# Kernel tuning notes

Hardware: AMD Instinct MI355X
Metric: run time of the kernel (lower is better)

The kernel has to match this reference:

```python
import jax, jax.numpy as jnp
import numpy as np

# opt hyperparameters (from init_kwargs)
L = 16        # number of multipath taps
M = 64        # number of subcarriers (FFT size for H_t)
N_PILOT = 2   # pilot symbols
V = 100.0     # velocity used for Doppler shift


def setup_inputs() -> dict:
    key = jax.random.key(0)
    k1, k2, k3, k4 = jax.random.split(key, 4)
    N, P, S, MK = 1024, 8, 14, 80
    SMK = S * MK  # 1120
    return {
        "input_real": jax.random.normal(k1, (N, P, SMK), dtype=jnp.float32),
        "input_imag": jax.random.normal(k2, (N, P, SMK), dtype=jnp.float32),
        "cof_real": jax.random.normal(k3, (N, P, L), dtype=jnp.float32),
        "cof_imag": jax.random.normal(k4, (N, P, L), dtype=jnp.float32),
        "Ns": 12,
    }


def reference(input_real, input_imag, cof_real, cof_imag, Ns):
    N, P, SMK = input_real.shape
    S = Ns + N_PILOT
    x = (input_real + 1j * input_imag).astype(jnp.complex64)   # (N,P,SMK)
    cof = (cof_real + 1j * cof_imag).astype(jnp.complex64)      # (N,P,L)

    # H_t: FFT of zero-padded channel taps along delay dim
    cof_zp = jnp.concatenate([cof, jnp.zeros((N, P, M - L), dtype=cof.dtype)], axis=-1)
    H_t = jnp.fft.fft(cof_zp, axis=-1)                          # (N,P,M)

    # Doppler phase shifts: shift[l,s] = exp(i * 2*pi*cos(angle_l)*fd * t_s)
    t = jnp.linspace(0.0, (S - 1) * (0.0005 / 14.0), S)         # (S,)
    carrier_freq = 3.0e9
    max_doppler = V / 3.0e8 * carrier_freq
    angles = jnp.linspace(0.0, 2.0 * np.pi, L)                  # (L,)
    phases = jnp.outer(2.0 * np.pi * jnp.cos(angles) * max_doppler, t)  # (L,S)
    shift = jnp.exp(1j * phases).astype(jnp.complex64)          # (L,S)

    # out[n,p,s,k] = sum_l x[n,p,s,k] * cof[n,p,l] * shift[l,s]
    # The sum over L factors out of the MK dim -> fused weight, avoiding the
    # (N,P,L,S,MK) broadcast intermediate the original materializes.
    weight = jnp.einsum('npl,ls->nps', cof, shift)              # (N,P,S)
    out = x.reshape(N, P, S, -1) * weight[..., None]            # (N,P,S,MK)
    output = out.reshape(N, P, SMK)
    return output, H_t
```

## Files before the change

kernel.cpp:

```cpp
#include <hip/hip_runtime.h>
#include <math.h>

#define L_TAPS 16
#define M_FFT  64
#define ROWS   4
#define SMAX   128

__global__ __launch_bounds__(256) void channel_fused(
    const float* __restrict__ xr, const float* __restrict__ xi,
    const float* __restrict__ cr, const float* __restrict__ ci,
    const int*   __restrict__ ns_ptr,
    float* __restrict__ out,
    int NP, int SMK)
{
    __shared__ float2 s_tw[M_FFT];
    __shared__ float  s_dop[L_TAPS];
    __shared__ float2 s_cof[ROWS][L_TAPS];
    __shared__ float2 s_w[ROWS * SMAX];

    const int tid  = threadIdx.x;
    const int S    = ns_ptr[0] + 2;
    const int MK   = SMK / S;
    const int row0 = blockIdx.x * ROWS;

    const float two_pi = 6.2831853071795864f;

    if (tid < M_FFT) {
        float sp, cp;
        __sincosf(-(float)tid * (two_pi / (float)M_FFT), &sp, &cp);
        s_tw[tid] = make_float2(cp, sp);
    } else if (tid < M_FFT + L_TAPS) {
        int l = tid - M_FFT;
        s_dop[l] = two_pi * __cosf((float)l * (two_pi / (float)(L_TAPS - 1)))
                 * (100.0f / 3.0e8f * 3.0e9f);
    } else if (tid >= 128 && tid < 128 + ROWS * L_TAPS) {
        int r = (tid - 128) >> 4, l = tid & 15;
        int npp = row0 + r;
        if (npp < NP)
            s_cof[r][l] = make_float2(cr[(size_t)npp * L_TAPS + l],
                                      ci[(size_t)npp * L_TAPS + l]);
    }
    __syncthreads();

    if (S <= SMAX) {
        const int l = tid & 15;
        for (int s = tid >> 4; s < S; s += 16) {
            float sp, cp;
            __sincosf(s_dop[l] * ((float)s * (0.0005f / 14.0f)), &sp, &cp);
            #pragma unroll
            for (int r = 0; r < ROWS; ++r) {
                float2 c = s_cof[r][l];
                float pr = c.x * cp - c.y * sp;
                float pi_ = c.x * sp + c.y * cp;
                #pragma unroll
                for (int off = 8; off; off >>= 1) {
                    pr  += __shfl_xor(pr,  off, 16);
                    pi_ += __shfl_xor(pi_, off, 16);
                }
                if (l == 0 && row0 + r < NP) s_w[r * S + s] = make_float2(pr, pi_);
            }
        }
    }

    {
        const int r = tid >> 6, m = tid & 63;
        const int npp = row0 + r;
        if (npp < NP) {
            float hr = 0.f;
            #pragma unroll
            for (int l = 0; l < L_TAPS; ++l) {
                float2 c = s_cof[r][l];
                float2 t = s_tw[(m * l) & (M_FFT - 1)];
                hr += c.x * t.x - c.y * t.y;
            }
            out[(size_t)NP * SMK + (size_t)npp * M_FFT + m] = hr;
        }
    }
    __syncthreads();

    const int rows_here = min(ROWS, NP - row0);
    if (S <= SMAX && (MK & 3) == 0 && (SMK & 3) == 0) {
        const int   mkq   = MK >> 2;
        const int   limit = (rows_here * SMK) >> 2;
        const size_t gb   = (size_t)row0 * (SMK >> 2);
        const float4* xr4 = (const float4*)xr + gb;
        const float4* xi4 = (const float4*)xi + gb;
        float4*       o4  = (float4*)out + gb;
        for (int v = tid; v < limit; v += 256) {
            float4 a = xr4[v];
            float4 b = xi4[v];
            float2 w = s_w[(unsigned)v / (unsigned)mkq];
            float4 r4;
            r4.x = a.x * w.x - b.x * w.y;
            r4.y = a.y * w.x - b.y * w.y;
            r4.z = a.z * w.x - b.z * w.y;
            r4.w = a.w * w.x - b.w * w.y;
            o4[v] = r4;
        }
    } else if (S <= SMAX) {
        const size_t gb = (size_t)row0 * SMK;
        const int limit = rows_here * SMK;
        for (int i = tid; i < limit; i += 256) {
            float2 w = s_w[(unsigned)i / (unsigned)MK];
            out[gb + i] = xr[gb + i] * w.x - xi[gb + i] * w.y;
        }
    } else {
        const size_t gb = (size_t)row0 * SMK;
        const int limit = rows_here * SMK;
        for (int i = tid; i < limit; i += 256) {
            int r = i / SMK, s = (i - r * SMK) / MK;
            float wr = 0.f, wi = 0.f;
            #pragma unroll
            for (int l = 0; l < L_TAPS; ++l) {
                float sp, cp;
                __sincosf(s_dop[l] * ((float)s * (0.0005f / 14.0f)), &sp, &cp);
                float2 c = s_cof[r][l];
                wr += c.x * cp - c.y * sp;
                wi += c.x * sp + c.y * cp;
            }
            out[gb + i] = xr[gb + i] * wr - xi[gb + i] * wi;
        }
    }
}

extern "C" void kernel_launch(void* const* d_in, const int* in_sizes, int n_in,
                              void* d_out, int out_size, void* d_ws, size_t ws_size,
                              hipStream_t stream) {
    const float* xr = (const float*)d_in[0];
    const float* xi = (const float*)d_in[1];
    const float* cr = (const float*)d_in[2];
    const float* ci = (const float*)d_in[3];
    const int*   ns = (const int*)  d_in[4];

    const int NP  = in_sizes[2] / L_TAPS;
    const int SMK = in_sizes[0] / NP;
    (void)d_ws; (void)ws_size; (void)out_size; (void)n_in;

    channel_fused<<<(NP + ROWS - 1) / ROWS, 256, 0, stream>>>(
        xr, xi, cr, ci, ns, (float*)d_out, NP, SMK);
}
```

Before: 25.59 us.

## Unroll streaming loop with nontemporal vector loads and per-thread weight computation

The main streaming loop is unrolled by four so each thread issues four independent vector loads of both input planes before computing. The loads and stores use nontemporal builtins to bypass cache retention. The Doppler weight computation moves from a shuffle-reduction across 16 lanes to a per-thread 16-tap loop on the upper half of the block, with the Doppler constants folded in at compile time. It also drops the shared Doppler table and restricts the fast path to full blocks. The risk is that the per-thread sincos loop lengthens the prologue before the barrier.

```diff
diff --git a/kernel.cpp b/kernel.cpp
--- a/kernel.cpp
+++ b/kernel.cpp
@@ -5,6 +5,8 @@
 #define M_FFT  64
 #define ROWS   4
 #define SMAX   128
+
+typedef float v4f __attribute__((ext_vector_type(4)));
 
 __global__ __launch_bounds__(256) void channel_fused(
     const float* __restrict__ xr, const float* __restrict__ xi,
@@ -14,7 +16,6 @@
     int NP, int SMK)
 {
     __shared__ float2 s_tw[M_FFT];
-    __shared__ float  s_dop[L_TAPS];
     __shared__ float2 s_cof[ROWS][L_TAPS];
     __shared__ float2 s_w[ROWS * SMAX];
 
@@ -22,49 +23,48 @@
     const int S    = ns_ptr[0] + 2;
     const int MK   = SMK / S;
     const int row0 = blockIdx.x * ROWS;
-
     const float two_pi = 6.2831853071795864f;
 
-    if (tid < M_FFT) {
-        float sp, cp;
-        __sincosf(-(float)tid * (two_pi / (float)M_FFT), &sp, &cp);
-        s_tw[tid] = make_float2(cp, sp);
-    } else if (tid < M_FFT + L_TAPS) {
-        int l = tid - M_FFT;
-        s_dop[l] = two_pi * __cosf((float)l * (two_pi / (float)(L_TAPS - 1)))
-                 * (100.0f / 3.0e8f * 3.0e9f);
-    } else if (tid >= 128 && tid < 128 + ROWS * L_TAPS) {
-        int r = (tid - 128) >> 4, l = tid & 15;
+    if (tid < ROWS * L_TAPS) {
+        int r = tid >> 4, l = tid & 15;
         int npp = row0 + r;
         if (npp < NP)
             s_cof[r][l] = make_float2(cr[(size_t)npp * L_TAPS + l],
                                       ci[(size_t)npp * L_TAPS + l]);
+    } else if (tid < 64 + M_FFT) {
+        int m = tid - 64;
+        float sp, cp;
+        __sincosf(-(float)m * (two_pi / (float)M_FFT), &sp, &cp);
+        s_tw[m] = make_float2(cp, sp);
     }
     __syncthreads();
 
-    if (S <= SMAX) {
-        const int l = tid & 15;
-        for (int s = tid >> 4; s < S; s += 16) {
-            float sp, cp;
-            __sincosf(s_dop[l] * ((float)s * (0.0005f / 14.0f)), &sp, &cp);
-            #pragma unroll
-            for (int r = 0; r < ROWS; ++r) {
-                float2 c = s_cof[r][l];
-                float pr = c.x * cp - c.y * sp;
-                float pi_ = c.x * sp + c.y * cp;
+    if (S <= SMAX && tid >= 128) {
+        for (int q = tid - 128; q < ROWS * S; q += 128) {
+            int r = q / S;
+            int s = q - r * S;
+            if (row0 + r < NP) {
+                float t = (float)s * (0.0005f / 14.0f);
+                float wr = 0.f, wi = 0.f;
                 #pragma unroll
-                for (int off = 8; off; off >>= 1) {
-                    pr  += __shfl_xor(pr,  off, 16);
-                    pi_ += __shfl_xor(pi_, off, 16);
+                for (int l = 0; l < L_TAPS; ++l) {
+                    float dop = two_pi
+                              * __cosf((float)l * (two_pi / (float)(L_TAPS - 1)))
+                              * 1000.0f;
+                    float sp, cp;
+                    __sincosf(dop * t, &sp, &cp);
+                    float2 c = s_cof[r][l];
+                    wr += c.x * cp - c.y * sp;
+                    wi += c.x * sp + c.y * cp;
                 }
-                if (l == 0 && row0 + r < NP) s_w[r * S + s] = make_float2(pr, pi_);
+                s_w[q] = make_float2(wr, wi);
             }
         }
     }
 
     {
-        const int r = tid >> 6, m = tid & 63;
-        const int npp = row0 + r;
+        int r = tid >> 6, m = tid & 63;
+        int npp = row0 + r;
         if (npp < NP) {
             float hr = 0.f;
             #pragma unroll
@@ -79,23 +79,49 @@
     __syncthreads();
 
     const int rows_here = min(ROWS, NP - row0);
-    if (S <= SMAX && (MK & 3) == 0 && (SMK & 3) == 0) {
-        const int   mkq   = MK >> 2;
-        const int   limit = (rows_here * SMK) >> 2;
-        const size_t gb   = (size_t)row0 * (SMK >> 2);
-        const float4* xr4 = (const float4*)xr + gb;
-        const float4* xi4 = (const float4*)xi + gb;
-        float4*       o4  = (float4*)out + gb;
-        for (int v = tid; v < limit; v += 256) {
-            float4 a = xr4[v];
-            float4 b = xi4[v];
-            float2 w = s_w[(unsigned)v / (unsigned)mkq];
-            float4 r4;
-            r4.x = a.x * w.x - b.x * w.y;
-            r4.y = a.y * w.x - b.y * w.y;
-            r4.z = a.z * w.x - b.z * w.y;
-            r4.w = a.w * w.x - b.w * w.y;
-            o4[v] = r4;
+    if (S <= SMAX && (MK & 3) == 0 && (SMK & 3) == 0 && rows_here == ROWS) {
+        const unsigned mkq = (unsigned)(MK >> 2);
+        const int nvr   = SMK >> 2;
+        const int limit = ROWS * nvr;
+        const size_t gb = (size_t)row0 * nvr;
+        const v4f* xr4 = (const v4f*)xr + gb;
+        const v4f* xi4 = (const v4f*)xi + gb;
+        v4f*       o4  = (v4f*)out + gb;
+        const int niters = limit >> 8;
+
+        int j = 0;
+        for (; j + 4 <= niters; j += 4) {
+            const int v0 = (j << 8) + tid, v1 = v0 + 256, v2 = v0 + 512, v3 = v0 + 768;
+            v4f a0 = __builtin_nontemporal_load(xr4 + v0);
+            v4f a1 = __builtin_nontemporal_load(xr4 + v1);
+            v4f a2 = __builtin_nontemporal_load(xr4 + v2);
+            v4f a3 = __builtin_nontemporal_load(xr4 + v3);
+            v4f b0 = __builtin_nontemporal_load(xi4 + v0);
+            v4f b1 = __builtin_nontemporal_load(xi4 + v1);
+            v4f b2 = __builtin_nontemporal_load(xi4 + v2);
+            v4f b3 = __builtin_nontemporal_load(xi4 + v3);
+            float2 w0 = s_w[(unsigned)v0 / mkq];
+            float2 w1 = s_w[(unsigned)v1 / mkq];
+            float2 w2 = s_w[(unsigned)v2 / mkq];
+            float2 w3 = s_w[(unsigned)v3 / mkq];
+            __builtin_nontemporal_store(a0 * w0.x - b0 * w0.y, o4 + v0);
+            __builtin_nontemporal_store(a1 * w1.x - b1 * w1.y, o4 + v1);
+            __builtin_nontemporal_store(a2 * w2.x - b2 * w2.y, o4 + v2);
+            __builtin_nontemporal_store(a3 * w3.x - b3 * w3.y, o4 + v3);
+        }
+        for (; j < niters; ++j) {
+            const int v = (j << 8) + tid;
+            v4f a = __builtin_nontemporal_load(xr4 + v);
+            v4f b = __builtin_nontemporal_load(xi4 + v);
+            float2 w = s_w[(unsigned)v / mkq];
+            __builtin_nontemporal_store(a * w.x - b * w.y, o4 + v);
+        }
+        const int t = (niters << 8) + tid;
+        if (t < limit) {
+            v4f a = __builtin_nontemporal_load(xr4 + t);
+            v4f b = __builtin_nontemporal_load(xi4 + t);
+            float2 w = s_w[(unsigned)t / mkq];
+            __builtin_nontemporal_store(a * w.x - b * w.y, o4 + t);
         }
     } else if (S <= SMAX) {
         const size_t gb = (size_t)row0 * SMK;
@@ -109,11 +135,15 @@
         const int limit = rows_here * SMK;
         for (int i = tid; i < limit; i += 256) {
             int r = i / SMK, s = (i - r * SMK) / MK;
+            float t = (float)s * (0.0005f / 14.0f);
             float wr = 0.f, wi = 0.f;
             #pragma unroll
             for (int l = 0; l < L_TAPS; ++l) {
+                float dop = two_pi
+                          * __cosf((float)l * (two_pi / (float)(L_TAPS - 1)))
+                          * 1000.0f;
                 float sp, cp;
-                __sincosf(s_dop[l] * ((float)s * (0.0005f / 14.0f)), &sp, &cp);
+                __sincosf(dop * t, &sp, &cp);
                 float2 c = s_cof[r][l];
                 wr += c.x * cp - c.y * sp;
                 wi += c.x * sp + c.y * cp;
```

New measurement: 24.60 us. 3.9% less time.

## Map one row per block with 320 threads and nontemporal vector I/O

Applied to the files above, without the earlier changes.

Restructures the kernel so each block handles a single (n,p) row: 280 threads each load one float4 of real and imaginary input up front, 64 threads compute the H_t FFT taps directly with sincos, and S threads compute per-symbol Doppler weights without shuffles. Loads are issued before the weight computation so memory latency overlaps the math, and nontemporal loads/stores are used for streaming data. This gives 8192 blocks instead of 2048 and removes shared twiddle/coef staging and one barrier. The cost is more blocks, repeated cof loads from global, and 40 idle lanes per block in the streaming phase.

```diff
diff --git a/kernel.cpp b/kernel.cpp
--- a/kernel.cpp
+++ b/kernel.cpp
@@ -3,120 +3,120 @@
 
 #define L_TAPS 16
 #define M_FFT  64
-#define ROWS   4
 #define SMAX   128
+#define BLOCK  320
 
-__global__ __launch_bounds__(256) void channel_fused(
+typedef float v4f __attribute__((ext_vector_type(4)));
+
+__global__ __launch_bounds__(BLOCK) void channel_fused(
     const float* __restrict__ xr, const float* __restrict__ xi,
     const float* __restrict__ cr, const float* __restrict__ ci,
     const int*   __restrict__ ns_ptr,
     float* __restrict__ out,
     int NP, int SMK)
 {
-    __shared__ float2 s_tw[M_FFT];
-    __shared__ float  s_dop[L_TAPS];
-    __shared__ float2 s_cof[ROWS][L_TAPS];
-    __shared__ float2 s_w[ROWS * SMAX];
+    __shared__ float2 s_w[SMAX];
 
-    const int tid  = threadIdx.x;
-    const int S    = ns_ptr[0] + 2;
-    const int MK   = SMK / S;
-    const int row0 = blockIdx.x * ROWS;
-
+    const int tid = threadIdx.x;
+    const int np  = blockIdx.x;
+    const int S   = ns_ptr[0] + 2;
+    const int MK  = SMK / S;
     const float two_pi = 6.2831853071795864f;
 
-    if (tid < M_FFT) {
-        float sp, cp;
-        __sincosf(-(float)tid * (two_pi / (float)M_FFT), &sp, &cp);
-        s_tw[tid] = make_float2(cp, sp);
-    } else if (tid < M_FFT + L_TAPS) {
-        int l = tid - M_FFT;
-        s_dop[l] = two_pi * __cosf((float)l * (two_pi / (float)(L_TAPS - 1)))
-                 * (100.0f / 3.0e8f * 3.0e9f);
-    } else if (tid >= 128 && tid < 128 + ROWS * L_TAPS) {
-        int r = (tid - 128) >> 4, l = tid & 15;
-        int npp = row0 + r;
-        if (npp < NP)
-            s_cof[r][l] = make_float2(cr[(size_t)npp * L_TAPS + l],
-                                      ci[(size_t)npp * L_TAPS + l]);
-    }
-    __syncthreads();
+    const float* crow = cr + (size_t)np * L_TAPS;
+    const float* cirow = ci + (size_t)np * L_TAPS;
 
-    if (S <= SMAX) {
-        const int l = tid & 15;
-        for (int s = tid >> 4; s < S; s += 16) {
-            float sp, cp;
-            __sincosf(s_dop[l] * ((float)s * (0.0005f / 14.0f)), &sp, &cp);
-            #pragma unroll
-            for (int r = 0; r < ROWS; ++r) {
-                float2 c = s_cof[r][l];
-                float pr = c.x * cp - c.y * sp;
-                float pi_ = c.x * sp + c.y * cp;
-                #pragma unroll
-                for (int off = 8; off; off >>= 1) {
-                    pr  += __shfl_xor(pr,  off, 16);
-                    pi_ += __shfl_xor(pi_, off, 16);
-                }
-                if (l == 0 && row0 + r < NP) s_w[r * S + s] = make_float2(pr, pi_);
-            }
+    const int nvr = SMK >> 2;
+    const bool fast = ((MK & 3) == 0) && ((SMK & 3) == 0) && (nvr <= BLOCK) && (S <= SMAX);
+
+    if (fast) {
+        const size_t gb = (size_t)np * nvr;
+        const bool act = tid < nvr;
+        v4f a, b;
+        if (act) {
+            a = __builtin_nontemporal_load((const v4f*)xr + gb + tid);
+            b = __builtin_nontemporal_load((const v4f*)xi + gb + tid);
         }
-    }
-
-    {
-        const int r = tid >> 6, m = tid & 63;
-        const int npp = row0 + r;
-        if (npp < NP) {
+        if (tid >= BLOCK - 64) {
+            const int m = tid - (BLOCK - 64);
             float hr = 0.f;
             #pragma unroll
             for (int l = 0; l < L_TAPS; ++l) {
-                float2 c = s_cof[r][l];
-                float2 t = s_tw[(m * l) & (M_FFT - 1)];
-                hr += c.x * t.x - c.y * t.y;
+                float sp, cp;
+                __sincosf((float)((m * l) & (M_FFT - 1)) * (two_pi / (float)M_FFT), &sp, &cp);
+                hr += crow[l] * cp + cirow[l] * sp;
             }
-            out[(size_t)NP * SMK + (size_t)npp * M_FFT + m] = hr;
+            __builtin_nontemporal_store(
+                hr, out + (size_t)NP * SMK + (size_t)np * M_FFT + m);
         }
+        if (tid < S) {
+            const float t = (float)tid * (0.0005f / 14.0f);
+            float wr = 0.f, wi = 0.f;
+            #pragma unroll
+            for (int l = 0; l < L_TAPS; ++l) {
+                float dop = two_pi * 1000.0f
+                          * __cosf((float)l * (two_pi / (float)(L_TAPS - 1)));
+                float sp, cp;
+                __sincosf(dop * t, &sp, &cp);
+                wr += crow[l] * cp - cirow[l] * sp;
+                wi += crow[l] * sp + cirow[l] * cp;
+            }
+            s_w[tid] = make_float2(wr, wi);
+        }
+        __syncthreads();
+        if (act) {
+            float2 w = s_w[(unsigned)tid / (unsigned)(MK >> 2)];
+            __builtin_nontemporal_store(a * w.x - b * w.y, (v4f*)out + gb + tid);
+        }
+        return;
     }
-    __syncthreads();
 
-    const int rows_here = min(ROWS, NP - row0);
-    if (S <= SMAX && (MK & 3) == 0 && (SMK & 3) == 0) {
-        const int   mkq   = MK >> 2;
-        const int   limit = (rows_here * SMK) >> 2;
-        const size_t gb   = (size_t)row0 * (SMK >> 2);
-        const float4* xr4 = (const float4*)xr + gb;
-        const float4* xi4 = (const float4*)xi + gb;
-        float4*       o4  = (float4*)out + gb;
-        for (int v = tid; v < limit; v += 256) {
-            float4 a = xr4[v];
-            float4 b = xi4[v];
-            float2 w = s_w[(unsigned)v / (unsigned)mkq];
-            float4 r4;
-            r4.x = a.x * w.x - b.x * w.y;
-            r4.y = a.y * w.x - b.y * w.y;
-            r4.z = a.z * w.x - b.z * w.y;
-            r4.w = a.w * w.x - b.w * w.y;
-            o4[v] = r4;
+    if (tid >= BLOCK - 64) {
+        const int m = tid - (BLOCK - 64);
+        float hr = 0.f;
+        #pragma unroll
+        for (int l = 0; l < L_TAPS; ++l) {
+            float sp, cp;
+            __sincosf((float)((m * l) & (M_FFT - 1)) * (two_pi / (float)M_FFT), &sp, &cp);
+            hr += crow[l] * cp + cirow[l] * sp;
         }
-    } else if (S <= SMAX) {
-        const size_t gb = (size_t)row0 * SMK;
-        const int limit = rows_here * SMK;
-        for (int i = tid; i < limit; i += 256) {
+        out[(size_t)NP * SMK + (size_t)np * M_FFT + m] = hr;
+    }
+    if (S <= SMAX) {
+        if (tid < S) {
+            const float t = (float)tid * (0.0005f / 14.0f);
+            float wr = 0.f, wi = 0.f;
+            #pragma unroll
+            for (int l = 0; l < L_TAPS; ++l) {
+                float dop = two_pi * 1000.0f
+                          * __cosf((float)l * (two_pi / (float)(L_TAPS - 1)));
+                float sp, cp;
+                __sincosf(dop * t, &sp, &cp);
+                wr += crow[l] * cp - cirow[l] * sp;
+                wi += crow[l] * sp + cirow[l] * cp;
+            }
+            s_w[tid] = make_float2(wr, wi);
+        }
+        __syncthreads();
+        const size_t gb = (size_t)np * SMK;
+        for (int i = tid; i < SMK; i += BLOCK) {
             float2 w = s_w[(unsigned)i / (unsigned)MK];
             out[gb + i] = xr[gb + i] * w.x - xi[gb + i] * w.y;
         }
     } else {
-        const size_t gb = (size_t)row0 * SMK;
-        const int limit = rows_here * SMK;
-        for (int i = tid; i < limit; i += 256) {
-            int r = i / SMK, s = (i - r * SMK) / MK;
+        const size_t gb = (size_t)np * SMK;
+        for (int i = tid; i < SMK; i += BLOCK) {
+            int s = i / MK;
+            float t = (float)s * (0.0005f / 14.0f);
             float wr = 0.f, wi = 0.f;
             #pragma unroll
             for (int l = 0; l < L_TAPS; ++l) {
+                float dop = two_pi * 1000.0f
+                          * __cosf((float)l * (two_pi / (float)(L_TAPS - 1)));
                 float sp, cp;
-                __sincosf(s_dop[l] * ((float)s * (0.0005f / 14.0f)), &sp, &cp);
-                float2 c = s_cof[r][l];
-                wr += c.x * cp - c.y * sp;
-                wi += c.x * sp + c.y * cp;
+                __sincosf(dop * t, &sp, &cp);
+                wr += crow[l] * cp - cirow[l] * sp;
+                wi += crow[l] * sp + cirow[l] * cp;
             }
             out[gb + i] = xr[gb + i] * wr - xi[gb + i] * wi;
         }
@@ -136,6 +136,6 @@
     const int SMK = in_sizes[0] / NP;
     (void)d_ws; (void)ws_size; (void)out_size; (void)n_in;
 
-    channel_fused<<<(NP + ROWS - 1) / ROWS, 256, 0, stream>>>(
-        xr, xi, cr, ci, ns, (float*)d_out, NP, SMK);
+    channel_fused<<<NP, BLOCK, 0, stream>>>(xr, xi, cr, ci, ns,
+                                            (float*)d_out, NP, SMK);
 }
```

Result: slower. 46.62 us (+82.2%).
